# Kernel optimization log

Hardware: AMD Instinct MI355X
Metric: run time of the kernel (lower is better)

The kernel has to match this reference:

```python
import jax, jax.numpy as jnp
import numpy as np

BETA = 0.5        # membrane decay (from source)
THRESHOLD = 1.0   # snn.Leaky default
ALPHA = 2.0       # ATan surrogate default slope (snntorch)


@jax.custom_vjp
def spike_fn(v):
    # Heaviside spike: 1 where membrane - threshold > 0
    return (v > 0).astype(v.dtype)


def _spike_fwd(v):
    return spike_fn(v), v


def _spike_bwd(v, g):
    # snntorch ATan surrogate gradient: (alpha/2) / (1 + (pi/2*alpha*v)^2)
    grad = (ALPHA / 2.0) / (1.0 + (jnp.pi / 2.0 * ALPHA * v) ** 2)
    return (g * grad,)


spike_fn.defvjp(_spike_fwd, _spike_bwd)


def setup_inputs() -> dict:
    key = jax.random.key(0)
    # x: [T, B, N] = [num_steps, batch, neurons]
    x = jax.random.normal(key, (128, 64, 4096), dtype=jnp.float32)
    return {"x": x}


def reference(x):
    # snntorch Leaky with init_hidden=True, reset_mechanism='subtract':
    #   reset_t = H(mem_{t-1} - thr)
    #   mem_t   = beta*mem_{t-1} + x_t - reset_t*thr
    #   spk_t   = H(mem_t - thr)
    mem0 = jnp.zeros(x.shape[1:], dtype=x.dtype)

    def step(mem, xt):
        reset = spike_fn(mem - THRESHOLD)
        mem_new = BETA * mem + xt - reset * THRESHOLD
        spk = spike_fn(mem_new - THRESHOLD)
        return mem_new, spk

    _, spk_rec = jax.lax.scan(step, mem0, x)  # spk_rec: [T, B, N]
    return spk_rec
```

## Files before the change

### kernel.cpp

```cpp
#include <hip/hip_runtime.h>


#define T_STEPS 128
#define D 24

__global__ __launch_bounds__(256) void snn_leaky_fwd(const float* __restrict__ x,
                                                     float* __restrict__ out,
                                                     int n) {
    const int idx = blockIdx.x * blockDim.x + threadIdx.x;
    if (idx >= n) return;

    const float* xp = x + idx;
    float* op = out + idx;

    float buf[D];
    float mem = 0.0f;

#pragma unroll
    for (int u = 0; u < D; ++u) buf[u] = xp[(size_t)u * n];

#pragma unroll
    for (int t = 0; t < T_STEPS; ++t) {
        const float v = buf[t % D];
        if (t + D < T_STEPS) {
            buf[t % D] = xp[(size_t)(t + D) * n];
        }
        mem = 0.5f * mem + v - (mem > 1.0f ? 1.0f : 0.0f);
        const float spk = (mem > 1.0f) ? 1.0f : 0.0f;
        __builtin_nontemporal_store(spk, op + (size_t)t * n);
    }
}

extern "C" void kernel_launch(void* const* d_in, const int* in_sizes, int n_in,
                              void* d_out, int out_size, void* d_ws, size_t ws_size,
                              hipStream_t stream) {
    const float* x = (const float*)d_in[0];
    float* out = (float*)d_out;

    const int total = in_sizes[0];
    const int n = total / T_STEPS;

    const int block = 256;
    const int grid = (n + block - 1) / block;
    snn_leaky_fwd<<<grid, block, 0, stream>>>(x, out, n);
}
```

Baseline: 233.8 us.

## Split into bit-packing recurrence kernel and vectorized float expansion kernel

The recurrence kernel now stores each neuron's spikes as four 32-bit bitmasks in the workspace instead of writing a float per time step. A second kernel expands those bits into float4 outputs, one block per time step and quarter, so the output writes are wide and coalesced. The fused kernel is kept as a fallback when the workspace is too small. The cost is an extra launch and a small workspace round trip, while the 134MB float output still has to be written.

```diff
diff --git a/kernel.cpp b/kernel.cpp
--- a/kernel.cpp
+++ b/kernel.cpp
@@ -1,20 +1,21 @@
 #include <hip/hip_runtime.h>
+#include <stdint.h>
 
 
 #define T_STEPS 128
+#define NWORDS 4
 #define D 24
 
-__global__ __launch_bounds__(256) void snn_leaky_fwd(const float* __restrict__ x,
-                                                     float* __restrict__ out,
-                                                     int n) {
+__global__ __launch_bounds__(256) void snn_pack(const float* __restrict__ x,
+                                                uint32_t* __restrict__ ws,
+                                                int n) {
     const int idx = blockIdx.x * blockDim.x + threadIdx.x;
     if (idx >= n) return;
-
     const float* xp = x + idx;
-    float* op = out + idx;
 
     float buf[D];
     float mem = 0.0f;
+    uint32_t w0 = 0, w1 = 0, w2 = 0, w3 = 0;
 
 #pragma unroll
     for (int u = 0; u < D; ++u) buf[u] = xp[(size_t)u * n];
@@ -22,9 +23,60 @@
 #pragma unroll
     for (int t = 0; t < T_STEPS; ++t) {
         const float v = buf[t % D];
-        if (t + D < T_STEPS) {
-            buf[t % D] = xp[(size_t)(t + D) * n];
-        }
+        if (t + D < T_STEPS) buf[t % D] = xp[(size_t)(t + D) * n];
+        mem = 0.5f * mem + v - (mem > 1.0f ? 1.0f : 0.0f);
+        const uint32_t bit = (mem > 1.0f) ? 1u : 0u;
+        if (t < 32)       w0 |= bit << (t & 31);
+        else if (t < 64)  w1 |= bit << (t & 31);
+        else if (t < 96)  w2 |= bit << (t & 31);
+        else              w3 |= bit << (t & 31);
+    }
+    ws[(size_t)0 * n + idx] = w0;
+    ws[(size_t)1 * n + idx] = w1;
+    ws[(size_t)2 * n + idx] = w2;
+    ws[(size_t)3 * n + idx] = w3;
+}
+
+__global__ __launch_bounds__(256) void snn_expand(const uint32_t* __restrict__ ws,
+                                                  float4* __restrict__ out,
+                                                  int n) {
+    const int t = blockIdx.x >> 2;
+    const int q = blockIdx.x & 3;
+    const int n4 = n >> 2;
+    const int span4 = n4 >> 2;
+    const int sh = t & 31;
+
+    const uint32_t* plane = ws + (size_t)(t >> 5) * n;
+    const uint4* wp4 = (const uint4*)plane + (size_t)q * span4;
+    float4* op = out + (size_t)t * n4 + (size_t)q * span4;
+
+    for (int i = threadIdx.x; i < span4; i += 256) {
+        const uint4 w = wp4[i];
+        float4 o;
+        o.x = (float)((w.x >> sh) & 1u);
+        o.y = (float)((w.y >> sh) & 1u);
+        o.z = (float)((w.z >> sh) & 1u);
+        o.w = (float)((w.w >> sh) & 1u);
+        op[i] = o;
+    }
+}
+
+__global__ __launch_bounds__(256) void snn_fused(const float* __restrict__ x,
+                                                 float* __restrict__ out,
+                                                 int n) {
+    const int idx = blockIdx.x * blockDim.x + threadIdx.x;
+    if (idx >= n) return;
+    const float* xp = x + idx;
+    float* op = out + idx;
+
+    float buf[D];
+    float mem = 0.0f;
+#pragma unroll
+    for (int u = 0; u < D; ++u) buf[u] = xp[(size_t)u * n];
+#pragma unroll
+    for (int t = 0; t < T_STEPS; ++t) {
+        const float v = buf[t % D];
+        if (t + D < T_STEPS) buf[t % D] = xp[(size_t)(t + D) * n];
         mem = 0.5f * mem + v - (mem > 1.0f ? 1.0f : 0.0f);
         const float spk = (mem > 1.0f) ? 1.0f : 0.0f;
         __builtin_nontemporal_store(spk, op + (size_t)t * n);
@@ -35,12 +87,16 @@
                               void* d_out, int out_size, void* d_ws, size_t ws_size,
                               hipStream_t stream) {
     const float* x = (const float*)d_in[0];
-    float* out = (float*)d_out;
-
     const int total = in_sizes[0];
     const int n = total / T_STEPS;
 
-    const int block = 256;
-    const int grid = (n + block - 1) / block;
-    snn_leaky_fwd<<<grid, block, 0, stream>>>(x, out, n);
+    const size_t ws_needed = (size_t)NWORDS * (size_t)n * sizeof(uint32_t);
+
+    if (ws_size >= ws_needed) {
+        uint32_t* ws = (uint32_t*)d_ws;
+        snn_pack<<<(n + 255) / 256, 256, 0, stream>>>(x, ws, n);
+        snn_expand<<<T_STEPS * 4, 256, 0, stream>>>(ws, (float4*)d_out, n);
+    } else {
+        snn_fused<<<(n + 255) / 256, 256, 0, stream>>>(x, (float*)d_out, n);
+    }
 }
```

Result: no change. 235.3 us (+0.6%).
